# Kernel optimization log

Measured on AMD Instinct MI355X. Metric: run time of the kernel, lower is better.

## Reference

```python
import jax, jax.numpy as jnp
import numpy as np

# dims
B, L, T, D = 8, 27, 256, 1152
GS = 3            # group_size
G = L // GS       # num_groups = 9
DD = 512          # downsample_dim
H, HD = 8, 64     # heads, head_dim
NQ = 1            # num_queries
OD = 2048         # output_dim
SCALE = 1.0 / float(np.sqrt(HD))


def setup_inputs() -> dict:
    key = jax.random.key(0)
    ks = jax.random.split(key, 12)
    s = 0.02
    return {
        "K": jax.random.normal(ks[0], (B, L, T, D), jnp.float32),
        "V": jax.random.normal(ks[1], (B, L, T, D), jnp.float32),
        # learnable queries: one (NQ, D) per layer, stacked -> (L, NQ, D)
        "query": jax.random.normal(ks[2], (L, NQ, D), jnp.float32),
        # per-group linear params (flax Linear: y = x @ W + b, W is (in, out))
        "Wq": jax.random.normal(ks[3], (G, D, DD), jnp.float32) * s,
        "bq": jnp.zeros((G, DD), jnp.float32),
        "Wk": jax.random.normal(ks[4], (G, D, DD), jnp.float32) * s,
        "bk": jnp.zeros((G, DD), jnp.float32),
        "Wv": jax.random.normal(ks[5], (G, D, DD), jnp.float32) * s,
        "bv": jnp.zeros((G, DD), jnp.float32),
        "Wo": jax.random.normal(ks[6], (G, DD, OD), jnp.float32) * s,
        "bo": jnp.zeros((G, OD), jnp.float32),
    }


def reference(K, V, query, Wq, bq, Wk, bk, Wv, bv, Wo, bo):
    # group the L layer axis: (B, G, GS, T, D); layers in a group share weights
    Kg = K.reshape(B, G, GS, T, D)
    Vg = V.reshape(B, G, GS, T, D)
    qg = query.reshape(G, GS, NQ, D)

    # projections (batched over groups; replaces L tiny per-layer linears)
    Qp = jnp.einsum('gsnd,gdf->gsnf', qg, Wq) + bq[:, None, None, :]
    Qp = Qp.reshape(G, GS, NQ, H, HD)
    Kp = (jnp.einsum('bgstd,gdf->bgstf', Kg, Wk)
          + bk[None, :, None, None, :]).reshape(B, G, GS, T, H, HD)
    Vp = (jnp.einsum('bgstd,gdf->bgstf', Vg, Wv)
          + bv[None, :, None, None, :]).reshape(B, G, GS, T, H, HD)

    # cross-attention: learnable query attends over T tokens per layer
    scores = jnp.einsum('gsnhe,bgsthe->bgsnht', Qp, Kp) * SCALE
    attn = jax.nn.softmax(scores, axis=-1)
    pooled = jnp.einsum('bgsnht,bgsthe->bgsnhe', attn, Vp)
    pooled = pooled.mean(axis=3)  # mean over queries (== squeeze when NQ=1) -> (B,G,GS,H,HD)

    # original does pooled.transpose(0,2,1).reshape(B, DD): head_dim-major flatten
    pooled = pooled.transpose(0, 1, 2, 4, 3).reshape(B, G, GS, DD)

    out = jnp.einsum('bgsf,gfo->bgso', pooled, Wo) + bo[None, :, None, :]
    return out.reshape(B, L, OD)
```

## Files before the change

### kernel.cpp

```cpp
#include <hip/hip_runtime.h>
#include <stdint.h>


__global__ __launch_bounds__(256) void qk_fused(
    const float* __restrict__ query, const float* __restrict__ Wq,
    const float* __restrict__ bq, const float* __restrict__ Wk,
    float* __restrict__ Qk)
{
  const int l = blockIdx.x, g = l / 3;
  const int h = blockIdx.y;
  const int dc = blockIdx.z;
  const int tid = threadIdx.x;

  __shared__ float qv[1152];
  __shared__ float part[4][64];
  __shared__ float Qps[64];

  for (int i = tid; i < 1152; i += 256) qv[i] = query[(size_t)l * 1152 + i];
  __syncthreads();

  {
    const int e = tid & 63;
    const int kq = tid >> 6;
    const float* W = Wq + (size_t)g * 1152 * 512 + h * 64 + e;
    float a0 = 0.f, a1 = 0.f;
    const int d0 = kq * 288;
#pragma unroll 4
    for (int d = d0; d < d0 + 288; d += 2) {
      a0 += qv[d]     * W[(size_t)d * 512];
      a1 += qv[d + 1] * W[(size_t)(d + 1) * 512];
    }
    part[kq][e] = a0 + a1;
  }
  __syncthreads();
  if (tid < 64) {
    const float r = part[0][tid] + part[1][tid] + part[2][tid] + part[3][tid];
    Qps[tid] = (r + bq[g * 512 + h * 64 + tid]) * 0.125f;
  }
  __syncthreads();

  const float4* q4base = (const float4*)Qps;
#pragma unroll
  for (int it = 0; it < 6; it++) {
    const int slot = it * 256 + tid;
    const int eg = slot & 3;
    const int d  = dc * 384 + (slot >> 2);
    const float4* q4 = q4base + eg * 4;
    const float4* w4 = (const float4*)(Wk + (size_t)g * 1152 * 512 + (size_t)d * 512 + h * 64 + eg * 16);
    float acc = 0.f;
#pragma unroll
    for (int e = 0; e < 4; e++) {
      const float4 a = q4[e], b = w4[e];
      acc += a.x * b.x + a.y * b.y + a.z * b.z + a.w * b.w;
    }
    acc += __shfl_xor(acc, 1, 64);
    acc += __shfl_xor(acc, 2, 64);
    if (eg == 0) Qk[((size_t)l * 1152 + d) * 8 + h] = acc;
  }
}

__global__ __launch_bounds__(256) void score_k(
    const float* __restrict__ K, const float* __restrict__ Qk,
    float* __restrict__ scores)
{
  const int bl = blockIdx.x;
  const int tq = blockIdx.y;
  const int l = bl % 27;
  const int tid = threadIdx.x;
  const int lane = tid & 63;
  const int wid = tid >> 6;

  __shared__ __align__(16) float Kt[96 * 65];
  __shared__ __align__(16) float Qs[96 * 8];

  const float* Kbase = K + ((size_t)bl * 256 + tq * 64) * 1152;
  const float* Qbase = Qk + (size_t)l * 1152 * 8;

  float sc[8] = {0.f, 0.f, 0.f, 0.f, 0.f, 0.f, 0.f, 0.f};

  for (int dc = 0; dc < 12; dc++) {
    __syncthreads();
#pragma unroll
    for (int it = 0; it < 6; it++) {
      const int flat = it * 256 + tid;
      const int row = flat / 24;
      const int col = flat % 24;
      const float4 v = *(const float4*)(Kbase + (size_t)row * 1152 + dc * 96 + col * 4);
      Kt[(col * 4 + 0) * 65 + row] = v.x;
      Kt[(col * 4 + 1) * 65 + row] = v.y;
      Kt[(col * 4 + 2) * 65 + row] = v.z;
      Kt[(col * 4 + 3) * 65 + row] = v.w;
    }
    if (tid < 192)
      ((float4*)Qs)[tid] = ((const float4*)(Qbase + (size_t)dc * 96 * 8))[tid];
    __syncthreads();

#pragma unroll 4
    for (int j = 0; j < 24; j++) {
      const int d = wid * 24 + j;
      const float kv = Kt[d * 65 + lane];
      const float4 qa = *(const float4*)&Qs[d * 8];
      const float4 qb = *(const float4*)&Qs[d * 8 + 4];
      sc[0] = fmaf(kv, qa.x, sc[0]); sc[1] = fmaf(kv, qa.y, sc[1]);
      sc[2] = fmaf(kv, qa.z, sc[2]); sc[3] = fmaf(kv, qa.w, sc[3]);
      sc[4] = fmaf(kv, qb.x, sc[4]); sc[5] = fmaf(kv, qb.y, sc[5]);
      sc[6] = fmaf(kv, qb.z, sc[6]); sc[7] = fmaf(kv, qb.w, sc[7]);
    }
  }

  __syncthreads();
  *(float4*)&Kt[(wid * 64 + lane) * 8    ] = make_float4(sc[0], sc[1], sc[2], sc[3]);
  *(float4*)&Kt[(wid * 64 + lane) * 8 + 4] = make_float4(sc[4], sc[5], sc[6], sc[7]);
  __syncthreads();
  for (int out = tid; out < 512; out += 256) {
    const int t = out >> 3, h = out & 7;
    const float s = (Kt[(0 * 64 + t) * 8 + h] + Kt[(1 * 64 + t) * 8 + h])
                  + (Kt[(2 * 64 + t) * 8 + h] + Kt[(3 * 64 + t) * 8 + h]);
    scores[((size_t)bl * 256 + tq * 64 + t) * 8 + h] = s;
  }
}

__global__ __launch_bounds__(384) void va_sm_k(
    const float* __restrict__ V, const float* __restrict__ scores,
    float* __restrict__ VA)
{
  const int bl = blockIdx.x;
  const int dt = blockIdx.y;
  const int tid = threadIdx.x;
  const int d  = dt * 384 + tid;

  __shared__ __align__(16) float at[2048];
  __shared__ float red[4][8], red2[4][8];

  const int wid = tid >> 6, lane = tid & 63;
  float sc[8], p[8];
  if (tid < 256) {
    const float* src = scores + ((size_t)bl * 256 + tid) * 8;
#pragma unroll
    for (int h = 0; h < 8; h++) sc[h] = src[h];
#pragma unroll
    for (int h = 0; h < 8; h++) {
      float m = sc[h];
#pragma unroll
      for (int o = 1; o < 64; o <<= 1) m = fmaxf(m, __shfl_xor(m, o, 64));
      if (lane == 0) red[wid][h] = m;
    }
  }
  __syncthreads();
  if (tid < 256) {
#pragma unroll
    for (int h = 0; h < 8; h++) {
      const float M = fmaxf(fmaxf(red[0][h], red[1][h]), fmaxf(red[2][h], red[3][h]));
      p[h] = __expf(sc[h] - M);
      float s = p[h];
#pragma unroll
      for (int o = 1; o < 64; o <<= 1) s += __shfl_xor(s, o, 64);
      if (lane == 0) red2[wid][h] = s;
    }
  }
  __syncthreads();
  if (tid < 256) {
#pragma unroll
    for (int h = 0; h < 8; h++) {
      const float S = red2[0][h] + red2[1][h] + red2[2][h] + red2[3][h];
      at[tid * 8 + h] = p[h] * (1.0f / S);
    }
  }
  __syncthreads();

  const float* Vbase = V + (size_t)bl * 256 * 1152 + d;
  float acc[8] = {0.f, 0.f, 0.f, 0.f, 0.f, 0.f, 0.f, 0.f};
#pragma unroll 4
  for (int t = 0; t < 256; t++) {
    const float v = Vbase[(size_t)t * 1152];
    const float4 a0 = *(const float4*)&at[t * 8];
    const float4 a1 = *(const float4*)&at[t * 8 + 4];
    acc[0] = fmaf(a0.x, v, acc[0]); acc[1] = fmaf(a0.y, v, acc[1]);
    acc[2] = fmaf(a0.z, v, acc[2]); acc[3] = fmaf(a0.w, v, acc[3]);
    acc[4] = fmaf(a1.x, v, acc[4]); acc[5] = fmaf(a1.y, v, acc[5]);
    acc[6] = fmaf(a1.z, v, acc[6]); acc[7] = fmaf(a1.w, v, acc[7]);
  }
  float* dst = VA + (size_t)bl * 8 * 1152 + d;
#pragma unroll
  for (int h = 0; h < 8; h++) dst[(size_t)h * 1152] = acc[h];
}

__global__ __launch_bounds__(512) void pv_mat(
    const float* __restrict__ VA, const float* __restrict__ Wv,
    float* __restrict__ psum)
{
  const int l = blockIdx.x, g = l / 3, h = blockIdx.y, dz = blockIdx.z;
  const int b = threadIdx.x >> 6, lane = threadIdx.x & 63;
  const int bl = b * 27 + l;
  const float* W = Wv + (size_t)g * 1152 * 512 + h * 64 + lane;
  const float* va = VA + ((size_t)bl * 8 + h) * 1152;
  const int d0 = dz * 288;
  float a0 = 0.f, a1 = 0.f, a2 = 0.f, a3 = 0.f;
#pragma unroll 2
  for (int d = d0; d < d0 + 288; d += 4) {
    a0 = fmaf(va[d],     W[(size_t)(d)     * 512], a0);
    a1 = fmaf(va[d + 1], W[(size_t)(d + 1) * 512], a1);
    a2 = fmaf(va[d + 2], W[(size_t)(d + 2) * 512], a2);
    a3 = fmaf(va[d + 3], W[(size_t)(d + 3) * 512], a3);
  }
  psum[((size_t)dz * 216 + bl) * 512 + lane * 8 + h] = (a0 + a1) + (a2 + a3);
}

__global__ __launch_bounds__(256) void out_gemm(
    const float* __restrict__ psum, const float* __restrict__ bv,
    const float* __restrict__ Wo, const float* __restrict__ bo,
    float* __restrict__ out)
{
  const int l = blockIdx.x, g = l / 3;
  const int n = blockIdx.y * 256 + threadIdx.x;
  __shared__ float pl[8][512];
  for (int i = threadIdx.x; i < 4096; i += 256) {
    const int b = i >> 9, f = i & 511;
    const int bl = b * 27 + l;
    const int e = f >> 3, h = f & 7;
    float v = bv[g * 512 + h * 64 + e];
#pragma unroll
    for (int dz = 0; dz < 4; dz++)
      v += psum[((size_t)dz * 216 + bl) * 512 + f];
    pl[b][f] = v;
  }
  __syncthreads();
  const float* W = Wo + (size_t)g * 512 * 2048 + n;
  float acc[8] = {0.f, 0.f, 0.f, 0.f, 0.f, 0.f, 0.f, 0.f};
#pragma unroll 4
  for (int f = 0; f < 512; f++) {
    const float w = W[(size_t)f * 2048];
#pragma unroll
    for (int b = 0; b < 8; b++) acc[b] += pl[b][f] * w;
  }
  const float bb = bo[g * 2048 + n];
#pragma unroll
  for (int b = 0; b < 8; b++)
    out[(size_t)(b * 27 + l) * 2048 + n] = acc[b] + bb;
}

__global__ __launch_bounds__(256) void zfill(float* __restrict__ out, int n) {
  const int i = blockIdx.x * 256 + threadIdx.x;
  if (i < n) out[i] = 0.f;
}

extern "C" void kernel_launch(void* const* d_in, const int* in_sizes, int n_in,
                              void* d_out, int out_size, void* d_ws, size_t ws_size,
                              hipStream_t stream)
{
  float* out = (float*)d_out;

  bool ok = (n_in == 11) && (out_size == 8 * 27 * 2048);
  if (ok) {
    const int expect[11] = {
      8 * 27 * 256 * 1152,
      8 * 27 * 256 * 1152,
      27 * 1 * 1152,
      9 * 1152 * 512,
      9 * 512,
      9 * 1152 * 512,
      9 * 512,
      9 * 1152 * 512,
      9 * 512,
      9 * 512 * 2048,
      9 * 2048
    };
    for (int i = 0; i < 11; i++) ok = ok && (in_sizes[i] == expect[i]);
  }
  const size_t NEED = 14321664;
  ok = ok && (ws_size >= NEED);

  if (!ok) {
    zfill<<<dim3((out_size + 255) / 256), dim3(256), 0, stream>>>(out, out_size);
    return;
  }

  const float* Kin   = (const float*)d_in[0];
  const float* Vin   = (const float*)d_in[1];
  const float* query = (const float*)d_in[2];
  const float* Wq    = (const float*)d_in[3];
  const float* bq    = (const float*)d_in[4];
  const float* Wk    = (const float*)d_in[5];
  const float* Wv    = (const float*)d_in[7];
  const float* bvp   = (const float*)d_in[8];
  const float* Wo    = (const float*)d_in[9];
  const float* bo    = (const float*)d_in[10];

  char* ws = (char*)d_ws;
  float* Qkw     = (float*)(ws + 55296);
  float* scoresw = (float*)(ws + 1050624);
  float* VAw     = (float*)(ws + 4589568);
  float* psumw   = (float*)(ws + 12552192);

  qk_fused<<<dim3(27, 8, 3), dim3(256), 0, stream>>>(query, Wq, bq, Wk, Qkw);
  score_k <<<dim3(216, 4),   dim3(256), 0, stream>>>(Kin, Qkw, scoresw);
  va_sm_k <<<dim3(216, 3),   dim3(384), 0, stream>>>(Vin, scoresw, VAw);
  pv_mat  <<<dim3(27, 8, 4), dim3(512), 0, stream>>>(VAw, Wv, psumw);
  out_gemm<<<dim3(27, 8),    dim3(256), 0, stream>>>(psumw, bvp, Wo, bo, out);
}
```

Measured before the change: 268.6 us.

## Fuse score and softmax-weighted V kernels into one per-(b,l) attention kernel

Merges the score kernel and the softmax/V-accumulation kernel into a single kernel with one 1024-thread block per (batch, layer). Scores stay in shared memory instead of going through a global buffer, and one launch is removed. The K-tile loads are register-prefetched one chunk ahead so they overlap the dot-product loop. In exchange, the grid shrinks to 216 large blocks, leaving some CUs idle. The score and V phases now run back to back inside each block, and the V columns are split unevenly across threads.

```diff
diff --git a/kernel.cpp b/kernel.cpp
--- a/kernel.cpp
+++ b/kernel.cpp
@@ -59,88 +59,91 @@
   }
 }
 
-__global__ __launch_bounds__(256) void score_k(
-    const float* __restrict__ K, const float* __restrict__ Qk,
-    float* __restrict__ scores)
+__global__ __launch_bounds__(1024) void attn_fused(
+    const float* __restrict__ K, const float* __restrict__ V,
+    const float* __restrict__ Qk, float* __restrict__ VA)
 {
   const int bl = blockIdx.x;
-  const int tq = blockIdx.y;
   const int l = bl % 27;
   const int tid = threadIdx.x;
   const int lane = tid & 63;
   const int wid = tid >> 6;
 
-  __shared__ __align__(16) float Kt[96 * 65];
-  __shared__ __align__(16) float Qs[96 * 8];
-
-  const float* Kbase = K + ((size_t)bl * 256 + tq * 64) * 1152;
+  __shared__ __align__(16) float Kt[192 * 65];
+  __shared__ __align__(16) float Qs[192 * 8];
+  __shared__ __align__(16) float sm[256 * 8];
+  __shared__ float red[4][8], red2[4][8];
+
   const float* Qbase = Qk + (size_t)l * 1152 * 8;
 
-  float sc[8] = {0.f, 0.f, 0.f, 0.f, 0.f, 0.f, 0.f, 0.f};
-
-  for (int dc = 0; dc < 12; dc++) {
+  for (int tq = 0; tq < 4; tq++) {
+    const float* Kbase = K + ((size_t)bl * 256 + tq * 64) * 1152;
+    float sc[8] = {0.f, 0.f, 0.f, 0.f, 0.f, 0.f, 0.f, 0.f};
+
+    float4 kreg[3]; float4 qreg;
+#pragma unroll
+    for (int it = 0; it < 3; it++) {
+      const int flat = it * 1024 + tid;
+      const int row = flat / 48, col = flat % 48;
+      kreg[it] = *(const float4*)(Kbase + (size_t)row * 1152 + col * 4);
+    }
+    if (tid < 384) qreg = ((const float4*)Qbase)[tid];
+
+    for (int dc = 0; dc < 6; dc++) {
+#pragma unroll
+      for (int it = 0; it < 3; it++) {
+        const int flat = it * 1024 + tid;
+        const int row = flat / 48, col = flat % 48;
+        Kt[(col * 4 + 0) * 65 + row] = kreg[it].x;
+        Kt[(col * 4 + 1) * 65 + row] = kreg[it].y;
+        Kt[(col * 4 + 2) * 65 + row] = kreg[it].z;
+        Kt[(col * 4 + 3) * 65 + row] = kreg[it].w;
+      }
+      if (tid < 384) ((float4*)Qs)[tid] = qreg;
+      __syncthreads();
+      if (dc + 1 < 6) {
+#pragma unroll
+        for (int it = 0; it < 3; it++) {
+          const int flat = it * 1024 + tid;
+          const int row = flat / 48, col = flat % 48;
+          kreg[it] = *(const float4*)(Kbase + (size_t)row * 1152 + (dc + 1) * 192 + col * 4);
+        }
+        if (tid < 384) qreg = ((const float4*)(Qbase + (size_t)(dc + 1) * 192 * 8))[tid];
+      }
+#pragma unroll 4
+      for (int j = 0; j < 12; j++) {
+        const int d = wid * 12 + j;
+        const float kv = Kt[d * 65 + lane];
+        const float4 qa = *(const float4*)&Qs[d * 8];
+        const float4 qb = *(const float4*)&Qs[d * 8 + 4];
+        sc[0] = fmaf(kv, qa.x, sc[0]); sc[1] = fmaf(kv, qa.y, sc[1]);
+        sc[2] = fmaf(kv, qa.z, sc[2]); sc[3] = fmaf(kv, qa.w, sc[3]);
+        sc[4] = fmaf(kv, qb.x, sc[4]); sc[5] = fmaf(kv, qb.y, sc[5]);
+        sc[6] = fmaf(kv, qb.z, sc[6]); sc[7] = fmaf(kv, qb.w, sc[7]);
+      }
+      __syncthreads();
+    }
+
+    *(float4*)&Kt[(wid * 64 + lane) * 8    ] = make_float4(sc[0], sc[1], sc[2], sc[3]);
+    *(float4*)&Kt[(wid * 64 + lane) * 8 + 4] = make_float4(sc[4], sc[5], sc[6], sc[7]);
     __syncthreads();
-#pragma unroll
-    for (int it = 0; it < 6; it++) {
-      const int flat = it * 256 + tid;
-      const int row = flat / 24;
-      const int col = flat % 24;
-      const float4 v = *(const float4*)(Kbase + (size_t)row * 1152 + dc * 96 + col * 4);
-      Kt[(col * 4 + 0) * 65 + row] = v.x;
-      Kt[(col * 4 + 1) * 65 + row] = v.y;
-      Kt[(col * 4 + 2) * 65 + row] = v.z;
-      Kt[(col * 4 + 3) * 65 + row] = v.w;
-    }
-    if (tid < 192)
-      ((float4*)Qs)[tid] = ((const float4*)(Qbase + (size_t)dc * 96 * 8))[tid];
+    if (tid < 512) {
+      const int t = tid >> 3, h = tid & 7;
+      float s = 0.f;
+#pragma unroll
+      for (int w = 0; w < 16; w++) s += Kt[(w * 64 + t) * 8 + h];
+      sm[(tq * 64 + t) * 8 + h] = s;
+    }
     __syncthreads();
-
-#pragma unroll 4
-    for (int j = 0; j < 24; j++) {
-      const int d = wid * 24 + j;
-      const float kv = Kt[d * 65 + lane];
-      const float4 qa = *(const float4*)&Qs[d * 8];
-      const float4 qb = *(const float4*)&Qs[d * 8 + 4];
-      sc[0] = fmaf(kv, qa.x, sc[0]); sc[1] = fmaf(kv, qa.y, sc[1]);
-      sc[2] = fmaf(kv, qa.z, sc[2]); sc[3] = fmaf(kv, qa.w, sc[3]);
-      sc[4] = fmaf(kv, qb.x, sc[4]); sc[5] = fmaf(kv, qb.y, sc[5]);
-      sc[6] = fmaf(kv, qb.z, sc[6]); sc[7] = fmaf(kv, qb.w, sc[7]);
-    }
-  }
-
-  __syncthreads();
-  *(float4*)&Kt[(wid * 64 + lane) * 8    ] = make_float4(sc[0], sc[1], sc[2], sc[3]);
-  *(float4*)&Kt[(wid * 64 + lane) * 8 + 4] = make_float4(sc[4], sc[5], sc[6], sc[7]);
-  __syncthreads();
-  for (int out = tid; out < 512; out += 256) {
-    const int t = out >> 3, h = out & 7;
-    const float s = (Kt[(0 * 64 + t) * 8 + h] + Kt[(1 * 64 + t) * 8 + h])
-                  + (Kt[(2 * 64 + t) * 8 + h] + Kt[(3 * 64 + t) * 8 + h]);
-    scores[((size_t)bl * 256 + tq * 64 + t) * 8 + h] = s;
-  }
-}
-
-__global__ __launch_bounds__(384) void va_sm_k(
-    const float* __restrict__ V, const float* __restrict__ scores,
-    float* __restrict__ VA)
-{
-  const int bl = blockIdx.x;
-  const int dt = blockIdx.y;
-  const int tid = threadIdx.x;
-  const int d  = dt * 384 + tid;
-
-  __shared__ __align__(16) float at[2048];
-  __shared__ float red[4][8], red2[4][8];
-
-  const int wid = tid >> 6, lane = tid & 63;
-  float sc[8], p[8];
+  }
+
+  float p[8], scl[8];
   if (tid < 256) {
-    const float* src = scores + ((size_t)bl * 256 + tid) * 8;
-#pragma unroll
-    for (int h = 0; h < 8; h++) sc[h] = src[h];
+#pragma unroll
+    for (int h = 0; h < 8; h++) scl[h] = sm[tid * 8 + h];
 #pragma unroll
     for (int h = 0; h < 8; h++) {
-      float m = sc[h];
+      float m = scl[h];
 #pragma unroll
       for (int o = 1; o < 64; o <<= 1) m = fmaxf(m, __shfl_xor(m, o, 64));
       if (lane == 0) red[wid][h] = m;
@@ -151,7 +154,7 @@
 #pragma unroll
     for (int h = 0; h < 8; h++) {
       const float M = fmaxf(fmaxf(red[0][h], red[1][h]), fmaxf(red[2][h], red[3][h]));
-      p[h] = __expf(sc[h] - M);
+      p[h] = __expf(scl[h] - M);
       float s = p[h];
 #pragma unroll
       for (int o = 1; o < 64; o <<= 1) s += __shfl_xor(s, o, 64);
@@ -163,26 +166,40 @@
 #pragma unroll
     for (int h = 0; h < 8; h++) {
       const float S = red2[0][h] + red2[1][h] + red2[2][h] + red2[3][h];
-      at[tid * 8 + h] = p[h] * (1.0f / S);
-    }
-  }
-  __syncthreads();
-
-  const float* Vbase = V + (size_t)bl * 256 * 1152 + d;
-  float acc[8] = {0.f, 0.f, 0.f, 0.f, 0.f, 0.f, 0.f, 0.f};
-#pragma unroll 4
+      sm[tid * 8 + h] = p[h] * (1.0f / S);
+    }
+  }
+  __syncthreads();
+
+  const float* Vbl = V + (size_t)bl * 256 * 1152;
+  const int d  = tid;
+  const int d2 = 1024 + tid;
+  const bool has2 = (tid < 128);
+  float acc[8]  = {0.f, 0.f, 0.f, 0.f, 0.f, 0.f, 0.f, 0.f};
+  float acc2[8] = {0.f, 0.f, 0.f, 0.f, 0.f, 0.f, 0.f, 0.f};
+#pragma unroll 8
   for (int t = 0; t < 256; t++) {
-    const float v = Vbase[(size_t)t * 1152];
-    const float4 a0 = *(const float4*)&at[t * 8];
-    const float4 a1 = *(const float4*)&at[t * 8 + 4];
+    const float v = Vbl[(size_t)t * 1152 + d];
+    const float4 a0 = *(const float4*)&sm[t * 8];
+    const float4 a1 = *(const float4*)&sm[t * 8 + 4];
     acc[0] = fmaf(a0.x, v, acc[0]); acc[1] = fmaf(a0.y, v, acc[1]);
     acc[2] = fmaf(a0.z, v, acc[2]); acc[3] = fmaf(a0.w, v, acc[3]);
     acc[4] = fmaf(a1.x, v, acc[4]); acc[5] = fmaf(a1.y, v, acc[5]);
     acc[6] = fmaf(a1.z, v, acc[6]); acc[7] = fmaf(a1.w, v, acc[7]);
-  }
-  float* dst = VA + (size_t)bl * 8 * 1152 + d;
-#pragma unroll
-  for (int h = 0; h < 8; h++) dst[(size_t)h * 1152] = acc[h];
+    if (has2) {
+      const float w = Vbl[(size_t)t * 1152 + d2];
+      acc2[0] = fmaf(a0.x, w, acc2[0]); acc2[1] = fmaf(a0.y, w, acc2[1]);
+      acc2[2] = fmaf(a0.z, w, acc2[2]); acc2[3] = fmaf(a0.w, w, acc2[3]);
+      acc2[4] = fmaf(a1.x, w, acc2[4]); acc2[5] = fmaf(a1.y, w, acc2[5]);
+      acc2[6] = fmaf(a1.z, w, acc2[6]); acc2[7] = fmaf(a1.w, w, acc2[7]);
+    }
+  }
+  float* dst = VA + (size_t)bl * 8 * 1152;
+#pragma unroll
+  for (int h = 0; h < 8; h++) {
+    dst[(size_t)h * 1152 + d] = acc[h];
+    if (has2) dst[(size_t)h * 1152 + d2] = acc2[h];
+  }
 }
 
 __global__ __launch_bounds__(512) void pv_mat(
@@ -287,14 +304,12 @@
   const float* bo    = (const float*)d_in[10];
 
   char* ws = (char*)d_ws;
-  float* Qkw     = (float*)(ws + 55296);
-  float* scoresw = (float*)(ws + 1050624);
-  float* VAw     = (float*)(ws + 4589568);
-  float* psumw   = (float*)(ws + 12552192);
-
-  qk_fused<<<dim3(27, 8, 3), dim3(256), 0, stream>>>(query, Wq, bq, Wk, Qkw);
-  score_k <<<dim3(216, 4),   dim3(256), 0, stream>>>(Kin, Qkw, scoresw);
-  va_sm_k <<<dim3(216, 3),   dim3(384), 0, stream>>>(Vin, scoresw, VAw);
-  pv_mat  <<<dim3(27, 8, 4), dim3(512), 0, stream>>>(VAw, Wv, psumw);
-  out_gemm<<<dim3(27, 8),    dim3(256), 0, stream>>>(psumw, bvp, Wo, bo, out);
-}
+  float* Qkw   = (float*)(ws + 55296);
+  float* VAw   = (float*)(ws + 4589568);
+  float* psumw = (float*)(ws + 12552192);
+
+  qk_fused  <<<dim3(27, 8, 3), dim3(256),  0, stream>>>(query, Wq, bq, Wk, Qkw);
+  attn_fused<<<dim3(216),      dim3(1024), 0, stream>>>(Kin, Vin, Qkw, VAw);
+  pv_mat    <<<dim3(27, 8, 4), dim3(512),  0, stream>>>(VAw, Wv, psumw);
+  out_gemm  <<<dim3(27, 8),    dim3(256),  0, stream>>>(psumw, bvp, Wo, bo, out);
+}
```

Measured after the change: 343.9 us. 28.0% more time.
